# Kernel optimization log

Measured on AMD Instinct MI355X. Metric: run time of the kernel, lower is better.

The kernel has to match this reference:

```python
import jax, jax.numpy as jnp
import numpy as np

B, S, L, D, H = 4, 4, 1024, 1024, 16  # batch, state_size, seq_len, d_model, num_heads
DEPTH = D // H
NEG = -1.0e9


def setup_inputs() -> dict:
    key = jax.random.key(0)
    ks = jax.random.split(key, 10)
    scale = 1.0 / np.sqrt(D)
    q = jax.random.normal(ks[0], (B, S, L, D), jnp.float32)
    k = jax.random.normal(ks[1], (B, S, L, D), jnp.float32)
    v = jax.random.normal(ks[2], (B, S, L, D), jnp.float32)
    mask = (jax.random.uniform(ks[3], (B, S, L, L)) < 0.1).astype(jnp.float32)
    wq = jax.random.normal(ks[4], (D, D), jnp.float32) * scale
    wk = jax.random.normal(ks[5], (D, D), jnp.float32) * scale
    wv = jax.random.normal(ks[6], (D, D), jnp.float32) * scale
    wo = jax.random.normal(ks[7], (D, D), jnp.float32) * scale
    bq = jnp.zeros((D,), jnp.float32)
    bk = jnp.zeros((D,), jnp.float32)
    bv = jnp.zeros((D,), jnp.float32)
    bo = jnp.zeros((D,), jnp.float32)
    return {"q": q, "k": k, "v": v, "mask": mask, "wq": wq, "bq": bq,
            "wk": wk, "bk": bk, "wv": wv, "bv": bv, "wo": wo, "bo": bo}


def _split_heads(x):
    # [B,S,L,D] -> [B,S,H,L,depth]
    b, s, l, _ = x.shape
    return x.reshape(b, s, l, H, DEPTH).transpose(0, 1, 3, 2, 4)


def reference(q, k, v, mask, wq, bq, wk, bk, wv, bv, wo, bo):
    qh = _split_heads(q @ wq + bq)
    kh = _split_heads(k @ wk + bk)
    vh = _split_heads(v @ wv + bv)
    # scaled dot-product attention, logits: [B,S,H,Lq,Lk]
    logits = jnp.einsum('bshqd,bshkd->bshqk', qh, kh) / jnp.sqrt(
        jnp.asarray(DEPTH, jnp.float32))
    logits = logits + mask[:, :, None, :, :] * NEG
    attn = jax.nn.softmax(logits, axis=-1)
    ctx = jnp.einsum('bshqk,bshkd->bshqd', attn, vh)
    # merge heads: [B,S,H,L,depth] -> [B,S,L,D]
    ctx = ctx.transpose(0, 1, 3, 2, 4).reshape(q.shape[0], q.shape[1], q.shape[2], D)
    out = ctx @ wo + bo
    attn_mean = attn.mean(axis=2)  # mean over heads -> [B,S,Lq,Lk]
    return out, attn_mean
```

## Files before the change

kernel.cpp:

```cpp
#include <hip/hip_runtime.h>

typedef _Float16 h16;
typedef _Float16 v8h __attribute__((ext_vector_type(8)));
typedef float    v4f __attribute__((ext_vector_type(4)));
typedef unsigned long long u64;

constexpr float QPRESCALE = 0.18033688f;

#define MFMA16(a,b,c) __builtin_amdgcn_mfma_f32_16x16x32_f16((a),(b),(c),0,0,0)

__device__ __forceinline__ float fexp2(float x) {
#if __has_builtin(__builtin_amdgcn_exp2f)
    return __builtin_amdgcn_exp2f(x);
#else
    return __expf(x * 0.69314718056f);
#endif
}
__device__ __forceinline__ float flog2(float x) {
#if __has_builtin(__builtin_amdgcn_logf)
    return __builtin_amdgcn_logf(x);
#else
    return __logf(x) * 1.44269504f;
#endif
}

__device__ __forceinline__ void gld16(const h16* g, const h16* l)
{
    __builtin_amdgcn_global_load_lds(
        (const __attribute__((address_space(1))) void*)g,
        (__attribute__((address_space(3))) void*)l, 16, 0, 0);
}

__global__ __launch_bounds__(256)
void cvt16(const float* __restrict__ x, h16* __restrict__ y)
{
    size_t i = ((size_t)blockIdx.x * 256 + threadIdx.x) * 4;
    float4 v = *(const float4*)(x + i);
    h16 o[4] = {(h16)v.x, (h16)v.y, (h16)v.z, (h16)v.w};
    *(uint2*)(y + i) = *(const uint2*)o;
}

__global__ __launch_bounds__(256)
void mkbits(const float* __restrict__ mask, u64* __restrict__ mb)
{
    size_t i = (size_t)blockIdx.x * 256 + threadIdx.x;
    float v = mask[i];
    u64 b = __ballot(v != 0.0f);
    if ((threadIdx.x & 63) == 0) mb[i >> 6] = b;
}

__global__ __launch_bounds__(256)
void wtrans(const float* __restrict__ W, h16* __restrict__ WT)
{
    __shared__ float Ts[64][65];
    const int tid = threadIdx.x;
    const int n0 = blockIdx.x * 64, k0 = blockIdx.y * 64;
    #pragma unroll
    for (int i = 0; i < 4; ++i) {
        int f = tid + i * 256; int r = f >> 4, c = (f & 15) * 4;
        float4 v = *(const float4*)(W + (size_t)(k0 + r) * 1024 + n0 + c);
        Ts[r][c] = v.x; Ts[r][c+1] = v.y; Ts[r][c+2] = v.z; Ts[r][c+3] = v.w;
    }
    __syncthreads();
    #pragma unroll
    for (int i = 0; i < 4; ++i) {
        int f = tid + i * 256; int r = f >> 4, c = (f & 15) * 4;
        h16 o[4];
        #pragma unroll
        for (int j = 0; j < 4; ++j) o[j] = (h16)Ts[c + j][r];
        *(uint2*)(WT + (size_t)(n0 + r) * 1024 + k0 + c) = *(const uint2*)o;
    }
}

__global__ __launch_bounds__(256)
void proj(const h16* __restrict__ A, const h16* __restrict__ BT,
          const float* __restrict__ bias, void* __restrict__ out, int mode)
{
    __shared__ h16 As[128 * 32];
    __shared__ h16 Bs[128 * 32];
    const int tid  = threadIdx.x;
    const int lane = tid & 63, wv = tid >> 6;
    const int quad = lane >> 4, l16 = lane & 15;
    const int m0 = blockIdx.y * 128, n0 = blockIdx.x * 128;
    const int wm = (wv & 1) * 64, wn = (wv >> 1) * 64;
    const int sr = wv * 16 + (lane >> 2);
    const int sc = (lane & 3) * 8;
    v4f acc[4][4] = {};
    for (int k0 = 0; k0 < 1024; k0 += 32) {
        #pragma unroll
        for (int i = 0; i < 2; ++i) {
            int r = i * 64 + sr;
            gld16(A  + (size_t)(m0 + r) * 1024 + k0 + sc, &As[i * 2048 + wv * 512]);
            gld16(BT + (size_t)(n0 + r) * 1024 + k0 + sc, &Bs[i * 2048 + wv * 512]);
        }
        __syncthreads();
        v8h af[4], bf[4];
        #pragma unroll
        for (int t = 0; t < 4; ++t) {
            af[t] = *(v8h*)&As[(wm + t*16 + l16) * 32 + quad * 8];
            bf[t] = *(v8h*)&Bs[(wn + t*16 + l16) * 32 + quad * 8];
        }
        #pragma unroll
        for (int mt = 0; mt < 4; ++mt)
            #pragma unroll
            for (int nt = 0; nt < 4; ++nt)
                acc[mt][nt] = MFMA16(af[mt], bf[nt], acc[mt][nt]);
        __syncthreads();
    }
    #pragma unroll
    for (int mt = 0; mt < 4; ++mt) {
        int mbase = m0 + wm + mt*16 + quad*4;
        #pragma unroll
        for (int nt = 0; nt < 4; ++nt) {
            int n = n0 + wn + nt*16 + l16;
            float bv = bias[n];
            #pragma unroll
            for (int r = 0; r < 4; ++r) {
                float y = acc[mt][nt][r] + bv;
                if (mode == 0) y *= QPRESCALE;
                int mm = mbase + r;
                int bs = mm >> 10, l = mm & 1023, h = n >> 6, d = n & 63;
                if (mode <= 1)
                    ((h16*)out)[(((size_t)bs*16 + h) * 1024 + l) * 64 + d] = (h16)y;
                else if (mode == 2)
                    ((h16*)out)[(((size_t)bs*16 + h) * 64 + d) * 1024 + l] = (h16)y;
                else
                    ((float*)out)[(size_t)mm * 1024 + n] = y;
            }
        }
    }
}

__global__ __launch_bounds__(256, 3)
void attn_ctx(const h16* __restrict__ qh, const h16* __restrict__ kh,
              const h16* __restrict__ vt, const u64* __restrict__ mbits,
              h16* __restrict__ ctx, float* __restrict__ Lst)
{
    __shared__ h16 Qs[128][68];
    __shared__ h16 Ks[64][68];
    __shared__ h16 Vs[64][68];
    __shared__ h16 Ps[128][68];
    const int tid  = threadIdx.x;
    const int lane = tid & 63, wv = tid >> 6;
    const int quad = lane >> 4, l16 = lane & 15;
    const int orig = blockIdx.x + (blockIdx.y << 8);
    const int slot = orig >> 3;
    const int bsh  = (orig & 7) + ((slot & 31) << 3);
    const int qb   = (slot >> 5) << 7;
    const int bs = bsh >> 4, h = bsh & 15;
    const int qw = wv * 32;
    const int fr = tid >> 3, fc = (tid & 7) * 8;

    uint4 rK0 = *(const uint4*)(kh + ((size_t)bsh*1024 + fr     ) * 64 + fc);
    uint4 rK1 = *(const uint4*)(kh + ((size_t)bsh*1024 + fr + 32) * 64 + fc);
    uint4 rV0 = *(const uint4*)(vt + ((size_t)bsh*64 + fr     ) * 1024 + fc);
    uint4 rV1 = *(const uint4*)(vt + ((size_t)bsh*64 + fr + 32) * 1024 + fc);

    #pragma unroll
    for (int i = 0; i < 4; ++i) {
        int f = tid + i * 256; int r = f >> 3, c = (f & 7) * 8;
        *(uint4*)&Qs[r][c] = *(const uint4*)(qh + ((size_t)bsh*1024 + qb + r) * 64 + c);
    }
    v8h bones;
    {
        h16 o = (l16 == 0) ? (h16)1.0f : (h16)0.0f;
        #pragma unroll
        for (int j = 0; j < 8; ++j) bones[j] = o;
    }
    const u64* mrb = mbits + ((size_t)bs*1024 + qb + qw + quad*4) * 16;

    v4f accp[2][4] = {};
    v4f accs[2] = {};
    for (int kt = 0; kt < 16; ++kt) {
        __syncthreads();
        *(uint4*)&Ks[fr     ][fc] = rK0;
        *(uint4*)&Ks[fr + 32][fc] = rK1;
        *(uint4*)&Vs[fr     ][fc] = rV0;
        *(uint4*)&Vs[fr + 32][fc] = rV1;
        if (kt < 15) {
            rK0 = *(const uint4*)(kh + ((size_t)bsh*1024 + (kt+1)*64 + fr     ) * 64 + fc);
            rK1 = *(const uint4*)(kh + ((size_t)bsh*1024 + (kt+1)*64 + fr + 32) * 64 + fc);
            rV0 = *(const uint4*)(vt + ((size_t)bsh*64 + fr     ) * 1024 + (kt+1)*64 + fc);
            rV1 = *(const uint4*)(vt + ((size_t)bsh*64 + fr + 32) * 1024 + (kt+1)*64 + fc);
        }
        __syncthreads();
        v4f s[2][4] = {};
        #pragma unroll
        for (int kc = 0; kc < 2; ++kc) {
            v8h aq[2], bk[4];
            aq[0] = *(v8h*)&Qs[qw      + l16][kc*32 + quad*8];
            aq[1] = *(v8h*)&Qs[qw + 16 + l16][kc*32 + quad*8];
            #pragma unroll
            for (int nt = 0; nt < 4; ++nt)
                bk[nt] = *(v8h*)&Ks[nt*16 + l16][kc*32 + quad*8];
            #pragma unroll
            for (int mt = 0; mt < 2; ++mt)
                #pragma unroll
                for (int nt = 0; nt < 4; ++nt)
                    s[mt][nt] = MFMA16(aq[mt], bk[nt], s[mt][nt]);
        }
        #pragma unroll
        for (int mt = 0; mt < 2; ++mt)
            #pragma unroll
            for (int r = 0; r < 4; ++r) {
                int ql = qw + mt*16 + quad*4 + r;
                u64 m64 = mrb[(mt*16 + r) * 16 + kt];
                uint lo = (uint)(m64 >> l16);
                uint hi = (uint)(m64 >> (l16 + 32));
                #pragma unroll
                for (int nt = 0; nt < 4; ++nt) {
                    uint b = (((nt & 2) ? hi : lo) >> ((nt & 1) * 16)) & 1u;
                    float p = b ? 0.0f : fexp2(s[mt][nt][r]);
                    Ps[ql][nt*16 + l16] = (h16)p;
                }
            }
        __syncthreads();
        #pragma unroll
        for (int kc = 0; kc < 2; ++kc) {
            v8h ap[2], bv[4];
            ap[0] = *(v8h*)&Ps[qw      + l16][kc*32 + quad*8];
            ap[1] = *(v8h*)&Ps[qw + 16 + l16][kc*32 + quad*8];
            #pragma unroll
            for (int nt = 0; nt < 4; ++nt)
                bv[nt] = *(v8h*)&Vs[nt*16 + l16][kc*32 + quad*8];
            #pragma unroll
            for (int mt = 0; mt < 2; ++mt) {
                accs[mt] = MFMA16(ap[mt], bones, accs[mt]);
                #pragma unroll
                for (int nt = 0; nt < 4; ++nt)
                    accp[mt][nt] = MFMA16(ap[mt], bv[nt], accp[mt][nt]);
            }
        }
    }
    float lq[8];
    #pragma unroll
    for (int mt = 0; mt < 2; ++mt)
        #pragma unroll
        for (int r = 0; r < 4; ++r)
            lq[mt*4 + r] = accs[mt][r];
    if (l16 == 0) {
        #pragma unroll
        for (int j = 0; j < 8; ++j)
            Lst[(size_t)bsh*1024 + qb + qw + (j >> 2)*16 + quad*4 + (j & 3)] = lq[j];
    }
    float rcp[8];
    #pragma unroll
    for (int j = 0; j < 8; ++j) {
        float l = __shfl(lq[j], quad * 16);
        rcp[j] = 1.0f / l;
    }
    #pragma unroll
    for (int mt = 0; mt < 2; ++mt)
        #pragma unroll
        for (int nt = 0; nt < 4; ++nt) {
            int dep = nt*16 + l16;
            #pragma unroll
            for (int r = 0; r < 4; ++r) {
                int ql = qw + mt*16 + quad*4 + r;
                float y = accp[mt][nt][r] * rcp[mt*4 + r];
                ctx[((size_t)bs*1024 + qb + ql) * 1024 + h*64 + dep] = (h16)y;
            }
        }
}

__global__ __launch_bounds__(256)
void attn_mean_k(const h16* __restrict__ qh, const h16* __restrict__ kh,
                 const u64* __restrict__ mbits, const float* __restrict__ Lst,
                 float* __restrict__ am)
{
    __shared__ h16 Qs[128][68];
    __shared__ h16 Ks[64][68];
    const int tid  = threadIdx.x;
    const int lane = tid & 63, wv = tid >> 6;
    const int quad = lane >> 4, l16 = lane & 15;
    const int orig = blockIdx.x + (blockIdx.y << 4) + (blockIdx.z << 7);
    const int slot = orig >> 3;
    const int bs   = (orig & 7) + ((slot & 1) << 3);
    const int rem  = slot >> 1;
    const int kt   = rem & 15;
    const int qb   = (rem >> 4) << 7;
    const int qw = wv * 32;
    u64 mrow[2][4];
    #pragma unroll
    for (int mt = 0; mt < 2; ++mt)
        #pragma unroll
        for (int r = 0; r < 4; ++r) {
            int ql = qw + mt*16 + quad*4 + r;
            mrow[mt][r] = mbits[((size_t)bs*1024 + qb + ql) * 16 + kt];
        }
    float acc[2][4][4] = {};
    for (int h = 0; h < 16; ++h) {
        const int bsh = bs * 16 + h;
        __syncthreads();
        #pragma unroll
        for (int i = 0; i < 4; ++i) {
            int f = tid + i * 256; int r = f >> 3, c = (f & 7) * 8;
            *(uint4*)&Qs[r][c] = *(const uint4*)(qh + ((size_t)bsh*1024 + qb + r) * 64 + c);
        }
        #pragma unroll
        for (int i = 0; i < 2; ++i) {
            int f = tid + i * 256; int r = f >> 3, c = (f & 7) * 8;
            *(uint4*)&Ks[r][c] = *(const uint4*)(kh + ((size_t)bsh*1024 + kt*64 + r) * 64 + c);
        }
        __syncthreads();
        v4f s[2][4] = {};
        #pragma unroll
        for (int kc = 0; kc < 2; ++kc) {
            v8h aq[2], bk[4];
            aq[0] = *(v8h*)&Qs[qw      + l16][kc*32 + quad*8];
            aq[1] = *(v8h*)&Qs[qw + 16 + l16][kc*32 + quad*8];
            #pragma unroll
            for (int nt = 0; nt < 4; ++nt)
                bk[nt] = *(v8h*)&Ks[nt*16 + l16][kc*32 + quad*8];
            #pragma unroll
            for (int mt = 0; mt < 2; ++mt)
                #pragma unroll
                for (int nt = 0; nt < 4; ++nt)
                    s[mt][nt] = MFMA16(aq[mt], bk[nt], s[mt][nt]);
        }
        float ll[8];
        #pragma unroll
        for (int mt = 0; mt < 2; ++mt)
            #pragma unroll
            for (int r = 0; r < 4; ++r)
                ll[mt*4+r] = flog2(Lst[(size_t)bsh*1024 + qb + qw + mt*16 + quad*4 + r]);
        #pragma unroll
        for (int mt = 0; mt < 2; ++mt)
            #pragma unroll
            for (int nt = 0; nt < 4; ++nt)
                #pragma unroll
                for (int r = 0; r < 4; ++r)
                    acc[mt][nt][r] += fexp2(s[mt][nt][r] - ll[mt*4+r]);
    }
    #pragma unroll
    for (int mt = 0; mt < 2; ++mt)
        #pragma unroll
        for (int r = 0; r < 4; ++r) {
            int ql = qw + mt*16 + quad*4 + r;
            uint lo = (uint)(mrow[mt][r] >> l16);
            uint hi = (uint)(mrow[mt][r] >> (l16 + 32));
            #pragma unroll
            for (int nt = 0; nt < 4; ++nt) {
                uint b = (((nt & 2) ? hi : lo) >> ((nt & 1) * 16)) & 1u;
                am[((size_t)bs*1024 + qb + ql) * 1024 + kt*64 + nt*16 + l16]
                    = b ? 0.0f : acc[mt][nt][r] * 0.0625f;
            }
        }
}

extern "C" void kernel_launch(void* const* d_in, const int* in_sizes, int n_in,
                              void* d_out, int out_size, void* d_ws, size_t ws_size,
                              hipStream_t stream)
{
    const float* q    = (const float*)d_in[0];
    const float* k    = (const float*)d_in[1];
    const float* v    = (const float*)d_in[2];
    const float* mask = (const float*)d_in[3];
    const float* wq   = (const float*)d_in[4];
    const float* bq   = (const float*)d_in[5];
    const float* wk   = (const float*)d_in[6];
    const float* bk   = (const float*)d_in[7];
    const float* wv   = (const float*)d_in[8];
    const float* bv   = (const float*)d_in[9];
    const float* wo   = (const float*)d_in[10];
    const float* bo   = (const float*)d_in[11];

    const size_t TEN = (size_t)16384 * 1024;
    char* w = (char*)d_ws;
    h16* qf  = (h16*)w;             w += TEN * 2;
    h16* kf  = (h16*)w;             w += TEN * 2;
    h16* vf  = (h16*)w;             w += TEN * 2;
    h16* wqT = (h16*)w;             w += (size_t)1024*1024*2;
    h16* wkT = (h16*)w;             w += (size_t)1024*1024*2;
    h16* wvT = (h16*)w;             w += (size_t)1024*1024*2;
    h16* woT = (h16*)w;             w += (size_t)1024*1024*2;
    h16* qhh = (h16*)w;             w += TEN * 2;
    h16* khh = (h16*)w;             w += TEN * 2;
    h16* vtt = (h16*)w;             w += TEN * 2;
    h16* ctx = (h16*)w;             w += TEN * 2;
    float* Lst = (float*)w;         w += (size_t)256 * 1024 * 4;
    u64* mbits = (u64*)w;

    float* out = (float*)d_out;
    float* am  = out + TEN;

    mkbits<<<65536, 256, 0, stream>>>(mask, mbits);
    cvt16<<<16384, 256, 0, stream>>>(q, qf);
    cvt16<<<16384, 256, 0, stream>>>(k, kf);
    cvt16<<<16384, 256, 0, stream>>>(v, vf);
    wtrans<<<dim3(16,16), 256, 0, stream>>>(wq, wqT);
    wtrans<<<dim3(16,16), 256, 0, stream>>>(wk, wkT);
    wtrans<<<dim3(16,16), 256, 0, stream>>>(wv, wvT);
    wtrans<<<dim3(16,16), 256, 0, stream>>>(wo, woT);
    proj<<<dim3(8,128), 256, 0, stream>>>(qf, wqT, bq, qhh, 0);
    proj<<<dim3(8,128), 256, 0, stream>>>(kf, wkT, bk, khh, 1);
    proj<<<dim3(8,128), 256, 0, stream>>>(vf, wvT, bv, vtt, 2);
    attn_ctx<<<dim3(256,8), 256, 0, stream>>>(qhh, khh, vtt, mbits, ctx, Lst);
    attn_mean_k<<<dim3(16,8,16), 256, 0, stream>>>(qhh, khh, mbits, Lst, am);
    proj<<<dim3(8,128), 256, 0, stream>>>(ctx, woT, bo, out, 3);
}
```

Baseline: 829.6 us.

## Prefetch next head's Q/K in attn_mean, drop barrier, remap blocks, precompute log2

The attn_mean kernel now preloads the next head's Q and K tiles into registers while the current head is computed, so global-load latency overlaps with the math. The attn_ctx kernel drops a block-wide barrier after the P tile is written, since each wave only reads back its own rows. It also stores log2 of the row sum, which removes that log from the 16-head loop in attn_mean. Both kernels remap block indices so that neighbouring blocks share heads or batch slices, which is meant to improve L2 locality. The cost is more registers for the prefetch buffers, which may lower occupancy.

Result: slower. 1.029 ms (+24.0%).

```diff
diff --git a/kernel.cpp b/kernel.cpp
--- a/kernel.cpp
+++ b/kernel.cpp
@@ -145,8 +145,8 @@
     const int quad = lane >> 4, l16 = lane & 15;
     const int orig = blockIdx.x + (blockIdx.y << 8);
     const int slot = orig >> 3;
-    const int bsh  = (orig & 7) + ((slot & 31) << 3);
-    const int qb   = (slot >> 5) << 7;
+    const int bsh  = (orig & 7) + ((slot >> 3) << 3);
+    const int qb   = (slot & 7) << 7;
     const int bs = bsh >> 4, h = bsh & 15;
     const int qw = wv * 32;
     const int fr = tid >> 3, fc = (tid & 7) * 8;
@@ -214,7 +214,6 @@
                     Ps[ql][nt*16 + l16] = (h16)p;
                 }
             }
-        __syncthreads();
         #pragma unroll
         for (int kc = 0; kc < 2; ++kc) {
             v8h ap[2], bv[4];
@@ -241,7 +240,8 @@
     if (l16 == 0) {
         #pragma unroll
         for (int j = 0; j < 8; ++j)
-            Lst[(size_t)bsh*1024 + qb + qw + (j >> 2)*16 + quad*4 + (j & 3)] = lq[j];
+            Lst[(size_t)bsh*1024 + qb + qw + (j >> 2)*16 + quad*4 + (j & 3)]
+                = flog2(lq[j]);
     }
     float rcp[8];
     #pragma unroll
@@ -275,10 +275,9 @@
     const int quad = lane >> 4, l16 = lane & 15;
     const int orig = blockIdx.x + (blockIdx.y << 4) + (blockIdx.z << 7);
     const int slot = orig >> 3;
-    const int bs   = (orig & 7) + ((slot & 1) << 3);
-    const int rem  = slot >> 1;
-    const int kt   = rem & 15;
-    const int qb   = (rem >> 4) << 7;
+    const int bs   = ((orig & 7) << 1) + (slot >> 7);
+    const int kt   = slot & 15;
+    const int qb   = ((slot >> 4) & 7) << 7;
     const int qw = wv * 32;
     u64 mrow[2][4];
     #pragma unroll
@@ -288,19 +287,33 @@
             int ql = qw + mt*16 + quad*4 + r;
             mrow[mt][r] = mbits[((size_t)bs*1024 + qb + ql) * 16 + kt];
         }
+    const int pr = tid >> 3, pc = (tid & 7) * 8;
+    uint4 rq[4], rk[2];
+    {
+        const size_t bsh0 = (size_t)bs * 16;
+        #pragma unroll
+        for (int i = 0; i < 4; ++i)
+            rq[i] = *(const uint4*)(qh + (bsh0*1024 + qb + pr + 32*i) * 64 + pc);
+        #pragma unroll
+        for (int i = 0; i < 2; ++i)
+            rk[i] = *(const uint4*)(kh + (bsh0*1024 + kt*64 + pr + 32*i) * 64 + pc);
+    }
     float acc[2][4][4] = {};
     for (int h = 0; h < 16; ++h) {
         const int bsh = bs * 16 + h;
         __syncthreads();
         #pragma unroll
-        for (int i = 0; i < 4; ++i) {
-            int f = tid + i * 256; int r = f >> 3, c = (f & 7) * 8;
-            *(uint4*)&Qs[r][c] = *(const uint4*)(qh + ((size_t)bsh*1024 + qb + r) * 64 + c);
-        }
-        #pragma unroll
-        for (int i = 0; i < 2; ++i) {
-            int f = tid + i * 256; int r = f >> 3, c = (f & 7) * 8;
-            *(uint4*)&Ks[r][c] = *(const uint4*)(kh + ((size_t)bsh*1024 + kt*64 + r) * 64 + c);
+        for (int i = 0; i < 4; ++i) *(uint4*)&Qs[pr + 32*i][pc] = rq[i];
+        #pragma unroll
+        for (int i = 0; i < 2; ++i) *(uint4*)&Ks[pr + 32*i][pc] = rk[i];
+        if (h < 15) {
+            const size_t bshn = (size_t)bsh + 1;
+            #pragma unroll
+            for (int i = 0; i < 4; ++i)
+                rq[i] = *(const uint4*)(qh + (bshn*1024 + qb + pr + 32*i) * 64 + pc);
+            #pragma unroll
+            for (int i = 0; i < 2; ++i)
+                rk[i] = *(const uint4*)(kh + (bshn*1024 + kt*64 + pr + 32*i) * 64 + pc);
         }
         __syncthreads();
         v4f s[2][4] = {};
@@ -323,7 +336,7 @@
         for (int mt = 0; mt < 2; ++mt)
             #pragma unroll
             for (int r = 0; r < 4; ++r)
-                ll[mt*4+r] = flog2(Lst[(size_t)bsh*1024 + qb + qw + mt*16 + quad*4 + r]);
+                ll[mt*4+r] = Lst[(size_t)bsh*1024 + qb + qw + mt*16 + quad*4 + r];
         #pragma unroll
         for (int mt = 0; mt < 2; ++mt)
             #pragma unroll
```
